# Optimization experiments

Hardware: AMD Instinct MI355X
Metric: run time of the kernel (lower is better)

## Reference

```python
import jax, jax.numpy as jnp
import numpy as np

B, T, D = 32, 1024, 1024
K, F = 8, 4096
E, RH = 64, 128
NUM_STAGES, NUM_VIEWS = 5, 4


def setup_inputs() -> dict:
    key = jax.random.key(0)
    ks = jax.random.split(key, 16)
    s = 0.02
    return {
        "x": jax.random.normal(ks[0], (B, T, D), dtype=jnp.float32),
        "stage_ids": jax.random.randint(ks[1], (B,), 0, NUM_STAGES),
        "view_ids": jax.random.randint(ks[2], (B,), 0, NUM_VIEWS),
        # router params
        "stage_emb": jax.random.normal(ks[3], (NUM_STAGES, E), dtype=jnp.float32) * s,
        "view_emb": jax.random.normal(ks[4], (NUM_VIEWS, E), dtype=jnp.float32) * s,
        "rw1": jax.random.normal(ks[5], (2 * E, RH), dtype=jnp.float32) * s,
        "rb1": jnp.zeros((RH,), dtype=jnp.float32),
        "rw2": jax.random.normal(ks[6], (RH, K), dtype=jnp.float32) * s,
        "rb2": jnp.zeros((K,), dtype=jnp.float32),
        # stacked expert FFN params
        "w1": jax.random.normal(ks[7], (K, D, F), dtype=jnp.float32) * s,
        "b1": jnp.zeros((K, F), dtype=jnp.float32),
        "w2": jax.random.normal(ks[8], (K, F, D), dtype=jnp.float32) * s,
        "b2": jnp.zeros((K, D), dtype=jnp.float32),
    }


def _moe_forward(x, stage_ids, view_ids, stage_emb, view_emb, rw1, rb1, rw2, rb2, w1, b1, w2, b2):
    # Router: per-sample stage/view embeddings -> MLP -> softmax over experts
    z = jnp.concatenate([stage_emb[stage_ids], view_emb[view_ids]], axis=-1)  # [B, 2E]
    logits = jax.nn.relu(z @ rw1 + rb1) @ rw2 + rb2  # [B, K]
    expert_probs = jax.nn.softmax(logits, axis=-1)
    selected_expert = jnp.argmax(expert_probs, axis=-1)  # [B]

    # Top-1 dispatch: gather the selected expert's weights per sample, then
    # run a single batched FFN (equivalent math to per-expert masked loop).
    w1s = w1[selected_expert]  # [B, D, F]
    b1s = b1[selected_expert]  # [B, F]
    w2s = w2[selected_expert]  # [B, F, D]
    b2s = b2[selected_expert]  # [B, D]
    h = jax.nn.gelu(jnp.einsum('btd,bdf->btf', x, w1s) + b1s[:, None, :], approximate=False)
    output = jnp.einsum('btf,bfd->btd', h, w2s) + b2s[:, None, :]  # [B, T, D]

    # Switch-style load-balance loss: K * sum_i f_i * P_i
    expert_mask = jax.nn.one_hot(selected_expert, K, dtype=jnp.float32)  # [B, K]
    f = expert_mask.mean(axis=0)
    P = expert_probs.mean(axis=0)
    load_balance_loss = K * jnp.sum(f * P)
    return output, expert_probs, selected_expert, load_balance_loss


def reference(x, stage_ids, view_ids, stage_emb, view_emb, rw1, rb1, rw2, rb2, w1, b1, w2, b2):
    return _moe_forward(x, stage_ids, view_ids, stage_emb, view_emb, rw1, rb1, rw2, rb2, w1, b1, w2, b2)
```

## Files before the change

kernel.cpp:

```cpp
#include <hip/hip_runtime.h>
#include <hip/hip_bf16.h>
#include <math.h>

#define BATCH 32
#define TSEQ 1024
#define DMODEL 1024
#define KEXP 8
#define FFFN 4096
#define EEMB 64
#define RHID 128
#define NSTAGE 5
#define NVIEW 4

typedef float f32x4 __attribute__((ext_vector_type(4)));
typedef __bf16 bf16x8 __attribute__((ext_vector_type(8)));

#define AS1C(p) ((const __attribute__((address_space(1))) unsigned int*)(p))
#define AS3(p)  ((__attribute__((address_space(3))) unsigned int*)(p))

__device__ __forceinline__ unsigned short f32_to_bf16_rne(float f) {
    union { float f; unsigned int u; } v; v.f = f;
    unsigned int u = v.u;
    unsigned int r = u + 0x7FFFu + ((u >> 16) & 1u);
    return (unsigned short)(r >> 16);
}

__device__ int resolve_id_one(const int* __restrict__ raw, int b, int hi, int is64) {
    int v = is64 ? raw[2 * b] : raw[b];
    return v < 0 ? 0 : (v >= hi ? hi - 1 : v);
}
__device__ int ids_are_64(const int* __restrict__ raw, int hi) {
    bool is64 = true;
    for (int i = 1; i < 32; i += 2) is64 = is64 && (raw[i] == 0);
    for (int i = 0; i < 32; i += 2) is64 = is64 && (raw[i] >= 0 && raw[i] < hi);
    return is64 ? 1 : 0;
}

__global__ __launch_bounds__(RHID) void router_probs_r21(
    const int* __restrict__ stage_ids,
    const int* __restrict__ view_ids,
    const float* __restrict__ stage_emb,
    const float* __restrict__ view_emb,
    const float* __restrict__ rw1,
    const float* __restrict__ rb1,
    const float* __restrict__ rw2,
    const float* __restrict__ rb2,
    float* __restrict__ out_probs,
    float* __restrict__ out_sel,
    int* __restrict__ sel_ws)
{
    const int b = blockIdx.x;
    const int t = threadIdx.x;
    __shared__ double z[2 * EEMB];
    __shared__ double h[RHID];
    __shared__ double lg[KEXP];
    __shared__ int sid_s, vid_s;
    if (t == 0) {
        const int s64 = ids_are_64(stage_ids, NSTAGE);
        const int v64 = ids_are_64(view_ids, NVIEW);
        sid_s = resolve_id_one(stage_ids, b, NSTAGE, s64);
        vid_s = resolve_id_one(view_ids, b, NVIEW, v64);
    }
    __syncthreads();
    const int sid = sid_s, vid = vid_s;
    z[t] = (t < EEMB) ? (double)stage_emb[sid * EEMB + t]
                      : (double)view_emb[vid * EEMB + (t - EEMB)];
    __syncthreads();
    double acc = (double)rb1[t];
    for (int i = 0; i < 2 * EEMB; ++i) acc += z[i] * (double)rw1[i * RHID + t];
    h[t] = fmax(acc, 0.0);
    __syncthreads();
    if (t < KEXP) {
        double a = (double)rb2[t];
        for (int i = 0; i < RHID; ++i) a += h[i] * (double)rw2[i * KEXP + t];
        lg[t] = a;
    }
    __syncthreads();
    if (t == 0) {
        double mx = lg[0]; int am = 0;
        for (int k = 1; k < KEXP; ++k) if (lg[k] > mx) { mx = lg[k]; am = k; }
        double p[KEXP]; double den = 0.0;
        for (int k = 0; k < KEXP; ++k) { p[k] = exp(lg[k] - mx); den += p[k]; }
        for (int k = 0; k < KEXP; ++k) out_probs[b * KEXP + k] = (float)(p[k] / den);
        out_sel[b] = (float)am;
        sel_ws[b] = am;
    }
}

__global__ void router_loss_r21(const float* __restrict__ probs,
                                const int* __restrict__ sel,
                                float* __restrict__ out_loss)
{
    if (threadIdx.x != 0) return;
    double loss = 0.0;
    for (int k = 0; k < KEXP; ++k) {
        double ps = 0.0; int fc = 0;
        for (int b = 0; b < BATCH; ++b) {
            ps += (double)probs[b * KEXP + k];
            fc += (sel[b] == k) ? 1 : 0;
        }
        loss += ((double)fc / (double)BATCH) * (ps / (double)BATCH);
    }
    out_loss[0] = (float)((double)KEXP * loss);
}

__global__ void cvt_f32_bf16_r21(const float* __restrict__ src,
                                 unsigned short* __restrict__ dst, size_t n)
{
    size_t i = (size_t)blockIdx.x * blockDim.x + threadIdx.x;
    size_t stride = (size_t)gridDim.x * blockDim.x;
    for (size_t j = i * 4; j < n; j += stride * 4) {
        float4 v = *(const float4*)(src + j);
        ushort4 o;
        o.x = f32_to_bf16_rne(v.x); o.y = f32_to_bf16_rne(v.y);
        o.z = f32_to_bf16_rne(v.z); o.w = f32_to_bf16_rne(v.w);
        *(ushort4*)(dst + j) = o;
    }
}

__global__ __launch_bounds__(512) void transpose_f32_bf16_r21(
    const float* __restrict__ src, unsigned short* __restrict__ dst, int R, int C)
{
    __shared__ float tile[64][65];
    const int e = blockIdx.z;
    const float* s = src + (size_t)e * R * C;
    unsigned short* d = dst + (size_t)e * R * C;
    const int c0 = blockIdx.x * 64, r0 = blockIdx.y * 64;
    const int tx = threadIdx.x, ty = threadIdx.y;
    #pragma unroll
    for (int i = 0; i < 64; i += 8)
        tile[ty + i][tx] = s[(size_t)(r0 + ty + i) * C + (c0 + tx)];
    __syncthreads();
    #pragma unroll
    for (int i = 0; i < 64; i += 8)
        d[(size_t)(c0 + ty + i) * R + (r0 + tx)] = f32_to_bf16_rne(tile[tx][ty + i]);
}


#define BM 128
#define BN 128
#define BK 64

template<int MODE, int OBF>
__global__ __launch_bounds__(256, 4) void gemm_bt_r21(
    const unsigned short* __restrict__ Aall,
    const unsigned short* __restrict__ BTall,
    const float* __restrict__ biasAll,
    void* __restrict__ OutV,
    const int* __restrict__ sel, int g0,
    int M, int N, int K)
{
    const int bz = blockIdx.z;
    int e = sel[g0 + bz];
    e = e < 0 ? 0 : (e >= KEXP ? KEXP - 1 : e);
    const unsigned short* A  = Aall + (size_t)bz * M * K;
    const unsigned short* BT = BTall + (size_t)e * (size_t)N * K;
    const float* bias = biasAll + (size_t)e * N;

    __shared__ __align__(16) unsigned short As[BM][BK];
    __shared__ __align__(16) unsigned short Bs[BN][BK];

    const int tid  = threadIdx.x;
    const int lane = tid & 63;
    const int wave = tid >> 6;
    const int wr = wave >> 1;
    const int wc = wave & 1;
    const int fr = lane & 15;
    const int fq = lane >> 4;
    const int swz = fr & 7;

    const int brow = blockIdx.y * BM;
    const int bcol = blockIdx.x * BN;

    const int srow = lane >> 3;
    const int scol = ((lane & 7) ^ (lane >> 3)) * 8;

    const f32x4 zero = {0.f, 0.f, 0.f, 0.f};
    f32x4 acc[4][4];
    #pragma unroll
    for (int m = 0; m < 4; ++m)
        #pragma unroll
        for (int n = 0; n < 4; ++n) acc[m][n] = zero;

    for (int k0 = 0; k0 < K; k0 += BK) {
        #pragma unroll
        for (int i = 0; i < 4; ++i) {
            const int r0 = i * 32 + wave * 8;
            const unsigned short* gA = A + (size_t)(brow + r0 + srow) * K + (k0 + scol);
            __builtin_amdgcn_global_load_lds(AS1C(gA), AS3(&As[r0][0]), 16, 0, 0);
        }
        #pragma unroll
        for (int i = 0; i < 4; ++i) {
            const int r0 = i * 32 + wave * 8;
            const unsigned short* gB = BT + (size_t)(bcol + r0 + srow) * K + (k0 + scol);
            __builtin_amdgcn_global_load_lds(AS1C(gB), AS3(&Bs[r0][0]), 16, 0, 0);
        }
        __syncthreads();

        bf16x8 af[4][2], bfr[4][2];
        #pragma unroll
        for (int m = 0; m < 4; ++m) {
            const int ra = wr * 64 + m * 16 + fr;
            #pragma unroll
            for (int ks = 0; ks < 2; ++ks) {
                const int ch = (ks * 4 + fq) ^ swz;
                af[m][ks] = *(const bf16x8*)(&As[ra][ch * 8]);
            }
        }
        #pragma unroll
        for (int n = 0; n < 4; ++n) {
            const int rb = wc * 64 + n * 16 + fr;
            #pragma unroll
            for (int ks = 0; ks < 2; ++ks) {
                const int ch = (ks * 4 + fq) ^ swz;
                bfr[n][ks] = *(const bf16x8*)(&Bs[rb][ch * 8]);
            }
        }

        #pragma unroll
        for (int ks = 0; ks < 2; ++ks)
            #pragma unroll
            for (int m = 0; m < 4; ++m)
                #pragma unroll
                for (int n = 0; n < 4; ++n)
                    acc[m][n] = __builtin_amdgcn_mfma_f32_16x16x32_bf16(af[m][ks], bfr[n][ks], acc[m][n], 0, 0, 0);

        __syncthreads();
    }

    #pragma unroll
    for (int m = 0; m < 4; ++m) {
        #pragma unroll
        for (int n = 0; n < 4; ++n) {
            #pragma unroll
            for (int r = 0; r < 4; ++r) {
                const int row = brow + wr * 64 + m * 16 + fq * 4 + r;
                const int col = bcol + wc * 64 + n * 16 + fr;
                float v = acc[m][n][r] + bias[col];
                if (MODE == 0) v = 0.5f * v * (1.0f + erff(v * 0.70710678118654752f));
                const size_t idx = (size_t)bz * M * N + (size_t)row * N + col;
                if (OBF) ((unsigned short*)OutV)[idx] = f32_to_bf16_rne(v);
                else     ((float*)OutV)[idx] = v;
            }
        }
    }
}

extern "C" void kernel_launch(void* const* d_in, const int* in_sizes, int n_in,
                              void* d_out, int out_size, void* d_ws, size_t ws_size,
                              hipStream_t stream)
{
    const float* x         = (const float*)d_in[0];
    const int*   stage_ids = (const int*)d_in[1];
    const int*   view_ids  = (const int*)d_in[2];
    const float* stage_emb = (const float*)d_in[3];
    const float* view_emb  = (const float*)d_in[4];
    const float* rw1       = (const float*)d_in[5];
    const float* rb1       = (const float*)d_in[6];
    const float* rw2       = (const float*)d_in[7];
    const float* rb2       = (const float*)d_in[8];
    const float* w1        = (const float*)d_in[9];
    const float* b1        = (const float*)d_in[10];
    const float* w2        = (const float*)d_in[11];
    const float* b2        = (const float*)d_in[12];

    float* out_f = (float*)d_out;
    const size_t OUT_ELEMS = (size_t)BATCH * TSEQ * DMODEL;

    const size_t MB64 = 67108864ull;
    char* ws = (char*)d_ws;
    int* sel_ws            = (int*)ws;
    unsigned short* x_bf   = (unsigned short*)(ws + 4096);
    unsigned short* w1T    = (unsigned short*)(ws + 4096 + MB64);
    unsigned short* w2T    = (unsigned short*)(ws + 4096 + 2 * MB64);
    unsigned short* h_bf   = (unsigned short*)(ws + 4096 + 3 * MB64);

    int grp = 1;
    {
        const size_t base = 4096 + 3 * MB64;
        const size_t avail = ws_size > base ? ws_size - base : 0;
        for (int g = 32; g >= 1; g >>= 1) {
            if ((size_t)g * TSEQ * FFFN * 2 <= avail) { grp = g; break; }
        }
    }

    router_probs_r21<<<BATCH, RHID, 0, stream>>>(stage_ids, view_ids, stage_emb, view_emb,
        rw1, rb1, rw2, rb2,
        out_f + OUT_ELEMS,
        out_f + OUT_ELEMS + BATCH * KEXP,
        sel_ws);
    router_loss_r21<<<1, 64, 0, stream>>>(out_f + OUT_ELEMS, sel_ws,
        out_f + OUT_ELEMS + BATCH * KEXP + BATCH);

    cvt_f32_bf16_r21<<<2048, 256, 0, stream>>>(x, x_bf, (size_t)BATCH * TSEQ * DMODEL);
    dim3 tb(64, 8);
    transpose_f32_bf16_r21<<<dim3(FFFN / 64, DMODEL / 64, KEXP), tb, 0, stream>>>(w1, w1T, DMODEL, FFFN);
    transpose_f32_bf16_r21<<<dim3(DMODEL / 64, FFFN / 64, KEXP), tb, 0, stream>>>(w2, w2T, FFFN, DMODEL);

    for (int g0 = 0; g0 < BATCH; g0 += grp) {
        gemm_bt_r21<0, 1><<<dim3(FFFN / BN, TSEQ / BM, grp), 256, 0, stream>>>(
            x_bf + (size_t)g0 * TSEQ * DMODEL, w1T, b1,
            (void*)h_bf, sel_ws, g0, TSEQ, FFFN, DMODEL);
        gemm_bt_r21<1, 0><<<dim3(DMODEL / BN, TSEQ / BM, grp), 256, 0, stream>>>(
            h_bf, w2T, b2,
            (void*)(out_f + (size_t)g0 * TSEQ * DMODEL), sel_ws, g0, TSEQ, DMODEL, FFFN);
    }
}
```

Measured before the change: 835.3 us.

## Replace GEMM with 256x256-tile, 8-wave, double-buffered prefetching kernel

The batched expert GEMM changes from 128x128 tiles with 4 waves to 256x256 tiles with 8 waves (512 threads). It double-buffers 128KB of LDS and issues the next K-tile's global_load_lds during the MFMA work, sequenced by explicit vmcnt waits, barriers and s_setprio. The goal is higher operand reuse per tile and hiding global-load latency behind the matrix cores. In exchange, LDS use limits each CU to one resident block, the larger tiles leave fewer blocks for the second GEMM, and the hand-written wait counts must stay exactly right to avoid reading stale data.

```diff
diff --git a/kernel.cpp b/kernel.cpp
--- a/kernel.cpp
+++ b/kernel.cpp
@@ -36,7 +36,7 @@
     return is64 ? 1 : 0;
 }
 
-__global__ __launch_bounds__(RHID) void router_probs_r21(
+__global__ __launch_bounds__(RHID) void router_probs_r22(
     const int* __restrict__ stage_ids,
     const int* __restrict__ view_ids,
     const float* __restrict__ stage_emb,
@@ -87,7 +87,7 @@
     }
 }
 
-__global__ void router_loss_r21(const float* __restrict__ probs,
+__global__ void router_loss_r22(const float* __restrict__ probs,
                                 const int* __restrict__ sel,
                                 float* __restrict__ out_loss)
 {
@@ -104,7 +104,7 @@
     out_loss[0] = (float)((double)KEXP * loss);
 }
 
-__global__ void cvt_f32_bf16_r21(const float* __restrict__ src,
+__global__ void cvt_f32_bf16_r22(const float* __restrict__ src,
                                  unsigned short* __restrict__ dst, size_t n)
 {
     size_t i = (size_t)blockIdx.x * blockDim.x + threadIdx.x;
@@ -118,7 +118,7 @@
     }
 }
 
-__global__ __launch_bounds__(512) void transpose_f32_bf16_r21(
+__global__ __launch_bounds__(512) void transpose_f32_bf16_r22(
     const float* __restrict__ src, unsigned short* __restrict__ dst, int R, int C)
 {
     __shared__ float tile[64][65];
@@ -137,12 +137,8 @@
 }
 
 
-#define BM 128
-#define BN 128
-#define BK 64
-
 template<int MODE, int OBF>
-__global__ __launch_bounds__(256, 4) void gemm_bt_r21(
+__global__ __launch_bounds__(512) void gemm_8p_r22(
     const unsigned short* __restrict__ Aall,
     const unsigned short* __restrict__ BTall,
     const float* __restrict__ biasAll,
@@ -157,84 +153,123 @@
     const unsigned short* BT = BTall + (size_t)e * (size_t)N * K;
     const float* bias = biasAll + (size_t)e * N;
 
-    __shared__ __align__(16) unsigned short As[BM][BK];
-    __shared__ __align__(16) unsigned short Bs[BN][BK];
+    __shared__ __align__(16) unsigned short lds[65536];
+    char* Lc = (char*)lds;
 
     const int tid  = threadIdx.x;
     const int lane = tid & 63;
     const int wave = tid >> 6;
-    const int wr = wave >> 1;
-    const int wc = wave & 1;
+    const int wr = wave >> 2;
+    const int wc = wave & 3;
     const int fr = lane & 15;
     const int fq = lane >> 4;
     const int swz = fr & 7;
 
-    const int brow = blockIdx.y * BM;
-    const int bcol = blockIdx.x * BN;
+    const int brow = blockIdx.y * 256;
+    const int bcol = blockIdx.x * 256;
 
     const int srow = lane >> 3;
     const int scol = ((lane & 7) ^ (lane >> 3)) * 8;
 
+    const int NT = K >> 6;
+
+    const int aSlot = wr * 16384;
+    const int bSlot = 32768 + (wc >> 1) * 16384;
+    const int c0off = ((0 + fq) ^ swz) * 16;
+    const int c1off = ((4 + fq) ^ swz) * 16;
+
     const f32x4 zero = {0.f, 0.f, 0.f, 0.f};
-    f32x4 acc[4][4];
+    f32x4 acc[8][4];
     #pragma unroll
-    for (int m = 0; m < 4; ++m)
+    for (int m = 0; m < 8; ++m)
         #pragma unroll
         for (int n = 0; n < 4; ++n) acc[m][n] = zero;
 
-    for (int k0 = 0; k0 < K; k0 += BK) {
+    auto STAGE = [&](int isB, int h, int t) {
+        const int kh = t << 6;
+        char* dbase = Lc + (t & 1) * 65536 + isB * 32768 + h * 16384 + wave * 1024;
+        const unsigned short* sbase = isB ? (BT + (size_t)(bcol + h * 128) * K)
+                                          : (A + (size_t)(brow + h * 128) * K);
         #pragma unroll
-        for (int i = 0; i < 4; ++i) {
-            const int r0 = i * 32 + wave * 8;
-            const unsigned short* gA = A + (size_t)(brow + r0 + srow) * K + (k0 + scol);
-            __builtin_amdgcn_global_load_lds(AS1C(gA), AS3(&As[r0][0]), 16, 0, 0);
-        }
+        for (int j = 0; j < 2; ++j) {
+            const unsigned short* g = sbase + (size_t)(j * 64 + wave * 8 + srow) * K + (kh + scol);
+            __builtin_amdgcn_global_load_lds(AS1C(g), AS3(dbase + j * 8192), 16, 0, 0);
+        }
+    };
+
+    STAGE(0, 0, 0); STAGE(0, 1, 0);
+    STAGE(1, 0, 0); STAGE(1, 1, 0);
+    if (NT > 1) { STAGE(1, 0, 1); STAGE(1, 1, 1); }
+    asm volatile("s_waitcnt vmcnt(4)" ::: "memory");
+    __builtin_amdgcn_s_barrier();
+    __builtin_amdgcn_sched_barrier(0);
+
+    bf16x8 bfr[4][2];
+
+    for (int t = 0; t < NT; ++t) {
+        const int buf = (t & 1) * 65536;
+        const int aB = buf + aSlot;
+        const int bB = buf + bSlot;
+
         #pragma unroll
-        for (int i = 0; i < 4; ++i) {
-            const int r0 = i * 32 + wave * 8;
-            const unsigned short* gB = BT + (size_t)(bcol + r0 + srow) * K + (k0 + scol);
-            __builtin_amdgcn_global_load_lds(AS1C(gB), AS3(&Bs[r0][0]), 16, 0, 0);
-        }
-        __syncthreads();
-
-        bf16x8 af[4][2], bfr[4][2];
-        #pragma unroll
-        for (int m = 0; m < 4; ++m) {
-            const int ra = wr * 64 + m * 16 + fr;
-            #pragma unroll
-            for (int ks = 0; ks < 2; ++ks) {
-                const int ch = (ks * 4 + fq) ^ swz;
-                af[m][ks] = *(const bf16x8*)(&As[ra][ch * 8]);
-            }
-        }
-        #pragma unroll
-        for (int n = 0; n < 4; ++n) {
-            const int rb = wc * 64 + n * 16 + fr;
-            #pragma unroll
-            for (int ks = 0; ks < 2; ++ks) {
-                const int ch = (ks * 4 + fq) ^ swz;
-                bfr[n][ks] = *(const bf16x8*)(&Bs[rb][ch * 8]);
-            }
-        }
-
-        #pragma unroll
-        for (int ks = 0; ks < 2; ++ks)
-            #pragma unroll
-            for (int m = 0; m < 4; ++m)
+        for (int q = 0; q < 4; ++q) {
+            bf16x8 af0k0, af0k1, af1k0, af1k1;
+            {
+                const int la0 = (2 * q + 0) * 16 + fr;
+                const int la1 = (2 * q + 1) * 16 + fr;
+                af0k0 = *(const bf16x8*)(Lc + aB + la0 * 128 + c0off);
+                af0k1 = *(const bf16x8*)(Lc + aB + la0 * 128 + c1off);
+                af1k0 = *(const bf16x8*)(Lc + aB + la1 * 128 + c0off);
+                af1k1 = *(const bf16x8*)(Lc + aB + la1 * 128 + c1off);
+            }
+            if (q == 0) {
+                #pragma unroll
+                for (int n = 0; n < 4; ++n) {
+                    const int lb = (wc & 1) * 64 + n * 16 + fr;
+                    bfr[n][0] = *(const bf16x8*)(Lc + bB + lb * 128 + c0off);
+                    bfr[n][1] = *(const bf16x8*)(Lc + bB + lb * 128 + c1off);
+                }
+            }
+            if (q == 0)      { if (t + 1 < NT) STAGE(0, 0, t + 1); }
+            else if (q == 1) { if (t + 1 < NT) STAGE(0, 1, t + 1); }
+            else if (q == 2) { if (t + 2 < NT) STAGE(1, 0, t + 2); }
+            else             { if (t + 2 < NT) STAGE(1, 1, t + 2); }
+            if (q == 3) {
+                if (t < NT - 2) asm volatile("s_waitcnt vmcnt(4)" ::: "memory");
+                else            asm volatile("s_waitcnt vmcnt(0)" ::: "memory");
+            }
+            __builtin_amdgcn_sched_barrier(0);
+            __builtin_amdgcn_s_barrier();
+            asm volatile("s_waitcnt lgkmcnt(0)" ::: "memory");
+            __builtin_amdgcn_sched_barrier(0);
+            __builtin_amdgcn_s_setprio(1);
+            {
+                const int m0 = 2 * q, m1 = 2 * q + 1;
                 #pragma unroll
                 for (int n = 0; n < 4; ++n)
-                    acc[m][n] = __builtin_amdgcn_mfma_f32_16x16x32_bf16(af[m][ks], bfr[n][ks], acc[m][n], 0, 0, 0);
-
-        __syncthreads();
+                    acc[m0][n] = __builtin_amdgcn_mfma_f32_16x16x32_bf16(af0k0, bfr[n][0], acc[m0][n], 0, 0, 0);
+                #pragma unroll
+                for (int n = 0; n < 4; ++n)
+                    acc[m1][n] = __builtin_amdgcn_mfma_f32_16x16x32_bf16(af1k0, bfr[n][0], acc[m1][n], 0, 0, 0);
+                #pragma unroll
+                for (int n = 0; n < 4; ++n)
+                    acc[m0][n] = __builtin_amdgcn_mfma_f32_16x16x32_bf16(af0k1, bfr[n][1], acc[m0][n], 0, 0, 0);
+                #pragma unroll
+                for (int n = 0; n < 4; ++n)
+                    acc[m1][n] = __builtin_amdgcn_mfma_f32_16x16x32_bf16(af1k1, bfr[n][1], acc[m1][n], 0, 0, 0);
+            }
+            __builtin_amdgcn_s_setprio(0);
+            __builtin_amdgcn_s_barrier();
+        }
     }
 
     #pragma unroll
-    for (int m = 0; m < 4; ++m) {
+    for (int m = 0; m < 8; ++m) {
         #pragma unroll
         for (int n = 0; n < 4; ++n) {
             #pragma unroll
             for (int r = 0; r < 4; ++r) {
-                const int row = brow + wr * 64 + m * 16 + fq * 4 + r;
+                const int row = brow + wr * 128 + m * 16 + fq * 4 + r;
                 const int col = bcol + wc * 64 + n * 16 + fr;
                 float v = acc[m][n][r] + bias[col];
                 if (MODE == 0) v = 0.5f * v * (1.0f + erff(v * 0.70710678118654752f));
@@ -284,24 +319,24 @@
         }
     }
 
-    router_probs_r21<<<BATCH, RHID, 0, stream>>>(stage_ids, view_ids, stage_emb, view_emb,
+    router_probs_r22<<<BATCH, RHID, 0, stream>>>(stage_ids, view_ids, stage_emb, view_emb,
         rw1, rb1, rw2, rb2,
         out_f + OUT_ELEMS,
         out_f + OUT_ELEMS + BATCH * KEXP,
         sel_ws);
-    router_loss_r21<<<1, 64, 0, stream>>>(out_f + OUT_ELEMS, sel_ws,
+    router_loss_r22<<<1, 64, 0, stream>>>(out_f + OUT_ELEMS, sel_ws,
         out_f + OUT_ELEMS + BATCH * KEXP + BATCH);
 
-    cvt_f32_bf16_r21<<<2048, 256, 0, stream>>>(x, x_bf, (size_t)BATCH * TSEQ * DMODEL);
+    cvt_f32_bf16_r22<<<2048, 256, 0, stream>>>(x, x_bf, (size_t)BATCH * TSEQ * DMODEL);
     dim3 tb(64, 8);
-    transpose_f32_bf16_r21<<<dim3(FFFN / 64, DMODEL / 64, KEXP), tb, 0, stream>>>(w1, w1T, DMODEL, FFFN);
-    transpose_f32_bf16_r21<<<dim3(DMODEL / 64, FFFN / 64, KEXP), tb, 0, stream>>>(w2, w2T, FFFN, DMODEL);
+    transpose_f32_bf16_r22<<<dim3(FFFN / 64, DMODEL / 64, KEXP), tb, 0, stream>>>(w1, w1T, DMODEL, FFFN);
+    transpose_f32_bf16_r22<<<dim3(DMODEL / 64, FFFN / 64, KEXP), tb, 0, stream>>>(w2, w2T, FFFN, DMODEL);
 
     for (int g0 = 0; g0 < BATCH; g0 += grp) {
-        gemm_bt_r21<0, 1><<<dim3(FFFN / BN, TSEQ / BM, grp), 256, 0, stream>>>(
+        gemm_8p_r22<0, 1><<<dim3(FFFN / 256, TSEQ / 256, grp), 512, 0, stream>>>(
             x_bf + (size_t)g0 * TSEQ * DMODEL, w1T, b1,
             (void*)h_bf, sel_ws, g0, TSEQ, FFFN, DMODEL);
-        gemm_bt_r21<1, 0><<<dim3(DMODEL / BN, TSEQ / BM, grp), 256, 0, stream>>>(
+        gemm_8p_r22<1, 0><<<dim3(DMODEL / 256, TSEQ / 256, grp), 512, 0, stream>>>(
             h_bf, w2T, b2,
             (void*)(out_f + (size_t)g0 * TSEQ * DMODEL), sel_ws, g0, TSEQ, DMODEL, FFFN);
     }
```

After: 783.0 us. 6.3% less time.
